# Kernel optimization log

Measured on AMD Instinct MI355X. Metric: run time of the kernel, lower is better.

Reference implementation:

```python
import jax, jax.numpy as jnp
import numpy as np

N = 10000; IN = 256; HID = 256; Z = 64; NC = 10; E = 320000
GAMMA = -0.5; ZETA = 1.1; TEMP = 0.5  # GlobalArgs.gamma/zeta, AttentionFusion.temperature


def _spmm(row, col, vals, x):
    # sparse [N,N] @ dense [N,D] via gather + segment-sum scatter
    return jax.ops.segment_sum(vals[:, None] * x[col], row, num_segments=N)


def _encode(x, row, col, vals, gcn_W, gcn_b, m1_W, m1_b, m2_W, m2_b, s1_W, s1_b, s2_W, s2_b):
    hidden = jax.nn.relu(_spmm(row, col, vals, x @ gcn_W + gcn_b))  # GCNLayer
    mean = jax.nn.relu(hidden @ m1_W + m1_b) @ m2_W + m2_b
    std = jax.nn.softplus(jax.nn.relu(hidden @ s1_W + s1_b) @ s2_W + s2_b)
    return mean, mean, std  # eval mode: z = x_mean


def _denoise(x, row, col, vals, nb_W, nb_b, sf_W, sf_b, att_W, att_b):
    h1 = jax.nn.relu(x[row] @ nb_W + nb_b)  # nblayers_0 on source feats
    h2 = jax.nn.relu(x[col] @ sf_W + sf_b)  # selflayers_0 on dest feats
    w = jnp.concatenate([h1, h2], axis=1) @ att_W + att_b  # [E,1] log_alpha
    gate = jax.nn.sigmoid(w[:, 0])  # eval-mode hard-concrete
    mask = jnp.clip(gate * (ZETA - GAMMA) + GAMMA, 0.0, 1.0)
    mv = vals * mask
    rowsum = jax.ops.segment_sum(mv, row, num_segments=N) + 1e-10
    d = jnp.clip(rowsum ** -0.5, 0.0, 10.0)
    norm_vals = mv * d[row] * d[col]
    l0 = jnp.mean(jax.nn.sigmoid(w - jnp.log(-GAMMA / ZETA)))
    return norm_vals, l0


def setup_inputs() -> dict:
    key = jax.random.key(0)
    ks = jax.random.split(key, 32)
    w = lambda k, s: jax.random.normal(k, s, jnp.float32) * 0.05
    inp = {}
    inp['x'] = jax.random.normal(ks[0], (N, IN), jnp.float32)
    inp['row'] = jax.random.randint(ks[1], (E,), 0, N)
    inp['col'] = jax.random.randint(ks[2], (E,), 0, N)
    inp['adj_vals'] = jax.random.uniform(ks[3], (E,), jnp.float32)
    inp['gcn_W'] = w(ks[4], (IN, HID)); inp['gcn_b'] = jnp.zeros((HID,), jnp.float32)
    inp['m1_W'] = w(ks[5], (HID, Z)); inp['m1_b'] = jnp.zeros((Z,), jnp.float32)
    inp['m2_W'] = w(ks[6], (Z, Z)); inp['m2_b'] = jnp.zeros((Z,), jnp.float32)
    inp['s1_W'] = w(ks[7], (HID, Z)); inp['s1_b'] = jnp.zeros((Z,), jnp.float32)
    inp['s2_W'] = w(ks[8], (Z, Z)); inp['s2_b'] = jnp.zeros((Z,), jnp.float32)
    inp['nb_W'] = w(ks[9], (IN, HID)); inp['nb_b'] = jnp.zeros((HID,), jnp.float32)
    inp['sf_W'] = w(ks[10], (IN, HID)); inp['sf_b'] = jnp.zeros((HID,), jnp.float32)
    inp['att_W'] = w(ks[11], (2 * HID, 1)); inp['att_b'] = jnp.zeros((1,), jnp.float32)
    inp['f1_W'] = w(ks[12], (Z, 32)); inp['f1_b'] = jnp.zeros((32,), jnp.float32)
    inp['f2_W'] = jnp.zeros((32, 1), jnp.float32)  # att[2].weight.fill_(0.0)
    inp['head_W'] = w(ks[13], (Z, NC)); inp['head_b'] = jnp.zeros((NC,), jnp.float32)
    inp['d1_W'] = w(ks[14], (Z, HID)); inp['d1_b'] = jnp.zeros((HID,), jnp.float32)
    inp['d2_W'] = w(ks[15], (HID, IN)); inp['d2_b'] = jnp.zeros((IN,), jnp.float32)
    return inp


def reference(x, row, col, adj_vals, gcn_W, gcn_b, m1_W, m1_b, m2_W, m2_b, s1_W, s1_b, s2_W, s2_b,
              nb_W, nb_b, sf_W, sf_b, att_W, att_b, f1_W, f1_b, f2_W, head_W, head_b,
              d1_W, d1_b, d2_W, d2_b):
    enc = (gcn_W, gcn_b, m1_W, m1_b, m2_W, m2_b, s1_W, s1_b, s2_W, s2_b)
    # generative view
    z_gen, mu, logstd = _encode(x, row, col, adj_vals, *enc)
    adj_logits = z_gen @ z_gen.T  # vgae_decoder
    # denoised view
    den_vals, l0_loss = _denoise(x, row, col, adj_vals, nb_W, nb_b, sf_W, sf_b, att_W, att_b)
    z_den, _, _ = _encode(x, row, col, den_vals, *enc)
    # attention fusion
    h = jnp.stack([z_gen, z_den], axis=1)  # [N,2,Z]
    score = jnp.tanh(h @ f1_W + f1_b) @ f2_W  # [N,2,1]
    weights = jax.nn.softmax(score / TEMP, axis=1)
    z_fused = jnp.sum(h * weights, axis=1)
    # heads (cluster_proj is identity)
    q_fused = jax.nn.softmax(z_fused @ head_W + head_b, axis=1)
    q_gen = jax.nn.softmax(z_gen @ head_W + head_b, axis=1)
    q_den = jax.nn.softmax(z_den @ head_W + head_b, axis=1)
    recon_den = jax.nn.relu(z_den @ d1_W + d1_b) @ d2_W + d2_b
    return (q_fused, q_gen, q_den, adj_logits, z_fused, mu, logstd, l0_loss, z_den, weights, recon_den)
```

## Files before the change

### kernel.cpp

```cpp
#include <hip/hip_runtime.h>
#include <math.h>

#define NN 10000
#define EE 320000

#define OQF  0LL
#define OQG  100000LL
#define OQD  200000LL
#define OADJ 300000LL
#define OZF  100300000LL
#define OMU  100940000LL
#define OLS  101580000LL
#define OL0  102220000LL
#define OZD  102220001LL
#define OWT  102860001LL
#define OREC 102880001LL

typedef short short8 __attribute__((ext_vector_type(8)));
typedef float f32x4 __attribute__((ext_vector_type(4)));

static __device__ __forceinline__ ushort f2bf(float f) {
  uint u = __float_as_uint(f);
  return (ushort)((u + 0x7fffu + ((u >> 16) & 1u)) >> 16);
}

__global__ __launch_bounds__(256) void k_prep(
    const float* __restrict__ x,
    const float* __restrict__ gcnW, const float* __restrict__ nbW,
    const float* __restrict__ sfW, const float* __restrict__ d1W,
    const float* __restrict__ d2W,
    ushort* __restrict__ XB, ushort* __restrict__ GWT, ushort* __restrict__ NWT,
    ushort* __restrict__ SWT, ushort* __restrict__ D1T, ushort* __restrict__ D2T)
{
  const int b = blockIdx.x;
  if (b < 2560) {
    const int i = b * 1024 + threadIdx.x * 4;
    if (i < NN * 256) {
      const float4 v = *(const float4*)(x + i);
      ushort4 u;
      u.x = f2bf(v.x); u.y = f2bf(v.y); u.z = f2bf(v.z); u.w = f2bf(v.w);
      *(ushort4*)(XB + i) = u;
    }
    return;
  }
  const int t2 = b - 2560;
  if (t2 < 1024) {
    const int m = t2 >> 8, n = t2 & 255, k = threadIdx.x;
    const float* src = (m == 0) ? gcnW : (m == 1) ? nbW : (m == 2) ? sfW : d2W;
    ushort* dst = (m == 0) ? GWT : (m == 1) ? NWT : (m == 2) ? SWT : D2T;
    dst[n * 256 + k] = f2bf(src[k * 256 + n]);
  } else {
    const int local = (t2 - 1024) * 256 + threadIdx.x;
    const int n = local >> 6, k = local & 63;
    D1T[n * 64 + k] = f2bf(d1W[k * 256 + n]);
  }
}

__global__ __launch_bounds__(256) void k_gin(
    const ushort* __restrict__ XB,
    const ushort* __restrict__ GWT, const ushort* __restrict__ NWT,
    const ushort* __restrict__ SWT,
    const float* __restrict__ gcnb, const float* __restrict__ nbb,
    const float* __restrict__ sfb, const float* __restrict__ attW,
    ushort* __restrict__ xwb, float* __restrict__ a1, float* __restrict__ a2)
{
  const int sel = blockIdx.y;
  const ushort* WT = (sel == 0) ? GWT : (sel == 1) ? NWT : SWT;
  const float* B = (sel == 0) ? gcnb : (sel == 1) ? nbb : sfb;
  const float* redw = attW + ((sel == 2) ? 256 : 0);
  float* redout = (sel == 1) ? a1 : a2;

  const int tid = threadIdx.x;
  const int wave = tid >> 6, lane = tid & 63;
  const int lr = lane & 15, lk = lane >> 4;
  const int i0 = blockIdx.x * 64;
  const int j0 = wave * 64;

  f32x4 acc[4][4];
#pragma unroll
  for (int ti = 0; ti < 4; ++ti)
#pragma unroll
    for (int tj = 0; tj < 4; ++tj) acc[ti][tj] = (f32x4){0.f, 0.f, 0.f, 0.f};

  const short8 z8 = {0, 0, 0, 0, 0, 0, 0, 0};
  for (int kk = 0; kk < 8; ++kk) {
    short8 a[4], bfr[4];
#pragma unroll
    for (int t = 0; t < 4; ++t) {
      const int ri = i0 + t * 16 + lr;
      a[t] = (ri < NN) ? *(const short8*)(XB + (size_t)ri * 256 + kk * 32 + lk * 8) : z8;
      bfr[t] = *(const short8*)(WT + (size_t)(j0 + t * 16 + lr) * 256 + kk * 32 + lk * 8);
    }
#pragma unroll
    for (int ti = 0; ti < 4; ++ti)
#pragma unroll
      for (int tj = 0; tj < 4; ++tj)
        acc[ti][tj] = __builtin_amdgcn_mfma_f32_16x16x32_bf16(a[ti], bfr[tj], acc[ti][tj], 0, 0, 0);
  }

  if (sel == 0) {
#pragma unroll
    for (int ti = 0; ti < 4; ++ti) {
      const int gi0 = i0 + ti * 16 + lk * 4;
#pragma unroll
      for (int tj = 0; tj < 4; ++tj) {
        const int gj = j0 + tj * 16 + lr;
        const float bv = B[gj];
#pragma unroll
        for (int r = 0; r < 4; ++r) {
          const int gi = gi0 + r;
          if (gi < NN) xwb[(size_t)gi * 256 + gj] = f2bf(acc[ti][tj][r] + bv);
        }
      }
    }
  } else {
    float bw[4], aw[4];
#pragma unroll
    for (int tj = 0; tj < 4; ++tj) {
      const int gj = j0 + tj * 16 + lr;
      bw[tj] = B[gj];
      aw[tj] = redw[gj];
    }
#pragma unroll
    for (int ti = 0; ti < 4; ++ti) {
      const int gi0 = i0 + ti * 16 + lk * 4;
#pragma unroll
      for (int r = 0; r < 4; ++r) {
        float s = 0.f;
#pragma unroll
        for (int tj = 0; tj < 4; ++tj)
          s += fmaxf(acc[ti][tj][r] + bw[tj], 0.f) * aw[tj];
#pragma unroll
        for (int m = 1; m < 16; m <<= 1) s += __shfl_xor(s, m, 64);
        const int gi = gi0 + r;
        if (lr == 0 && gi < NN) atomicAdd(&redout[gi], s);
      }
    }
  }
}

__global__ __launch_bounds__(256) void k_zzt(const ushort* __restrict__ ZB, float* __restrict__ C)
{
  const int tid = threadIdx.x;
  const int wave = tid >> 6, lane = tid & 63;
  const int lr = lane & 15, lk = lane >> 4;
  const int i0 = blockIdx.x * 128 + (wave >> 1) * 64;
  const int j0 = blockIdx.y * 128 + (wave & 1) * 64;
  short8 a[4][2], b[4][2];
  const short8 z8 = {0, 0, 0, 0, 0, 0, 0, 0};
#pragma unroll
  for (int t = 0; t < 4; ++t) {
    const int ri = i0 + t * 16 + lr;
    const int rj = j0 + t * 16 + lr;
#pragma unroll
    for (int kk = 0; kk < 2; ++kk) {
      a[t][kk] = (ri < NN) ? *(const short8*)(ZB + (size_t)ri * 64 + kk * 32 + lk * 8) : z8;
      b[t][kk] = (rj < NN) ? *(const short8*)(ZB + (size_t)rj * 64 + kk * 32 + lk * 8) : z8;
    }
  }
  f32x4 acc[4][4];
#pragma unroll
  for (int ti = 0; ti < 4; ++ti)
#pragma unroll
    for (int tj = 0; tj < 4; ++tj) {
      acc[ti][tj] = (f32x4){0.f, 0.f, 0.f, 0.f};
      acc[ti][tj] = __builtin_amdgcn_mfma_f32_16x16x32_bf16(a[ti][0], b[tj][0], acc[ti][tj], 0, 0, 0);
      acc[ti][tj] = __builtin_amdgcn_mfma_f32_16x16x32_bf16(a[ti][1], b[tj][1], acc[ti][tj], 0, 0, 0);
    }
#pragma unroll
  for (int ti = 0; ti < 4; ++ti) {
    const int gi0 = i0 + ti * 16 + lk * 4;
    if (gi0 >= NN) continue;
#pragma unroll
    for (int tj = 0; tj < 4; ++tj) {
      const int gj = j0 + tj * 16 + lr;
      if (gj >= NN) continue;
      float* cp = C + (size_t)gi0 * NN + gj;
#pragma unroll
      for (int r = 0; r < 4; ++r) cp[(size_t)r * NN] = acc[ti][tj][r];
    }
  }
}

__global__ __launch_bounds__(256) void k_denoise(
    const int* __restrict__ row, const int* __restrict__ col,
    const float* __restrict__ vals, const float* __restrict__ a1,
    const float* __restrict__ a2, const float* __restrict__ attb,
    float* __restrict__ mv, float* __restrict__ rsum, int* __restrict__ cnt,
    float* __restrict__ l0acc)
{
  const int e = blockIdx.x * 256 + threadIdx.x;
  const int r = row[e], c = col[e];
  const float w = a1[r] + a2[c] + attb[0];
  const float gate = 1.f / (1.f + expf(-w));
  const float mask = fminf(fmaxf(gate * 1.6f - 0.5f, 0.f), 1.f);
  const float m = vals[e] * mask;
  mv[e] = m;
  atomicAdd(&rsum[r], m);
  atomicAdd(&cnt[r], 1);
  float part = 1.f / (1.f + expf(-(w + 0.78845736f)));
#pragma unroll
  for (int off = 32; off > 0; off >>= 1) part += __shfl_down(part, off);
  __shared__ float sw[4];
  if ((threadIdx.x & 63) == 0) sw[threadIdx.x >> 6] = part;
  __syncthreads();
  if (threadIdx.x == 0) atomicAdd(l0acc, sw[0] + sw[1] + sw[2] + sw[3]);
}

__global__ __launch_bounds__(1024) void k_scan(const int* __restrict__ cnt, int* __restrict__ offs)
{
  __shared__ int part[1024];
  const int t = threadIdx.x;
  const int chunk = (NN + 1023) / 1024;
  const int base = t * chunk;
  int s = 0;
  for (int i = 0; i < chunk; ++i) { int idx = base + i; if (idx < NN) s += cnt[idx]; }
  part[t] = s;
  __syncthreads();
  for (int off = 1; off < 1024; off <<= 1) {
    int v = (t >= off) ? part[t - off] : 0;
    __syncthreads();
    part[t] += v;
    __syncthreads();
  }
  int run = (t == 0) ? 0 : part[t - 1];
  for (int i = 0; i < chunk; ++i) {
    int idx = base + i;
    if (idx < NN) { offs[idx] = run; run += cnt[idx]; }
  }
  if (t == 1023) offs[NN] = part[1023];
}

__global__ __launch_bounds__(256) void k_scatter(
    const int* __restrict__ row, const int* __restrict__ col,
    const float* __restrict__ vals, const float* __restrict__ mv,
    const float* __restrict__ rsum,
    const int* __restrict__ offs, int* __restrict__ posc,
    int* __restrict__ scol, float* __restrict__ sav, float* __restrict__ sdv)
{
  const int e = blockIdx.x * 256 + threadIdx.x;
  const int r = row[e], c = col[e];
  const float dr = fminf(rsqrtf(rsum[r] + 1e-10f), 10.f);
  const float dc = fminf(rsqrtf(rsum[c] + 1e-10f), 10.f);
  const int p = atomicAdd(&posc[r], 1);
  const int d = offs[r] + p;
  scol[d] = c;
  sav[d] = vals[e];
  sdv[d] = mv[e] * dr * dc;
}

__global__ __launch_bounds__(128) void k_spmm(
    const ushort* __restrict__ xwb, const int* __restrict__ scol,
    const float* __restrict__ sav, const float* __restrict__ sdv,
    const int* __restrict__ offs,
    float* __restrict__ h1, float* __restrict__ h2)
{
  const int n = blockIdx.x;
  const int c = threadIdx.x;
  const int s = offs[n], e = offs[n + 1];
  float a10 = 0.f, a11 = 0.f, a20 = 0.f, a21 = 0.f;
  for (int i = s; i < e; ++i) {
    const int cc = scol[i];
    const uint u = *(const uint*)(xwb + (size_t)cc * 256 + 2 * c);
    const float v0 = __uint_as_float(u << 16);
    const float v1 = __uint_as_float(u & 0xffff0000u);
    const float va = sav[i], vd = sdv[i];
    a10 = fmaf(va, v0, a10); a11 = fmaf(va, v1, a11);
    a20 = fmaf(vd, v0, a20); a21 = fmaf(vd, v1, a21);
  }
  float2* p1 = (float2*)(h1 + (size_t)n * 256 + 2 * c);
  float2* p2 = (float2*)(h2 + (size_t)n * 256 + 2 * c);
  *p1 = make_float2(fmaxf(a10, 0.f), fmaxf(a11, 0.f));
  *p2 = make_float2(fmaxf(a20, 0.f), fmaxf(a21, 0.f));
}

__global__ __launch_bounds__(256) void k_tail(
    const float* __restrict__ H1, const float* __restrict__ H2,
    const float* __restrict__ m1W, const float* __restrict__ m1b,
    const float* __restrict__ m2W, const float* __restrict__ m2b,
    const float* __restrict__ s1W, const float* __restrict__ s1b,
    const float* __restrict__ s2W, const float* __restrict__ s2b,
    float* __restrict__ out, float* __restrict__ zden,
    ushort* __restrict__ zbg, ushort* __restrict__ zbd)
{
  const int v = blockIdx.y;
  const float* A  = (v == 2) ? H2 : H1;
  const float* W1 = (v == 1) ? s1W : m1W;
  const float* B1 = (v == 1) ? s1b : m1b;
  const float* W2 = (v == 1) ? s2W : m2W;
  const float* B2 = (v == 1) ? s2b : m2b;

  __shared__ float As[16][68];
  __shared__ float Ws[16][68];
  __shared__ float Ts[64][68];
  __shared__ float W2s[64][68];

  const int tid = threadIdx.x;
  const int r0 = blockIdx.x << 6;
  const int ty = tid >> 4, tx = tid & 15;
  const int lr = tid >> 2, lk = (tid & 3) << 2;
  const int wk = tid >> 4, wc = (tid & 15) << 2;
  float acc[4][4] = {};
  for (int kb = 0; kb < 16; ++kb) {
    const int k0 = kb << 4;
    float4 av = make_float4(0.f, 0.f, 0.f, 0.f);
    const int gr = r0 + lr;
    if (gr < NN) av = *(const float4*)(A + (size_t)gr * 256 + k0 + lk);
    As[lk + 0][lr] = av.x; As[lk + 1][lr] = av.y;
    As[lk + 2][lr] = av.z; As[lk + 3][lr] = av.w;
    const float4 wv = *(const float4*)(W1 + (size_t)(k0 + wk) * 64 + wc);
    *(float4*)&Ws[wk][wc] = wv;
    __syncthreads();
#pragma unroll
    for (int k = 0; k < 16; ++k) {
      const float4 a = *(const float4*)&As[k][ty << 2];
      const float4 b = *(const float4*)&Ws[k][tx << 2];
      const float ar[4] = {a.x, a.y, a.z, a.w};
      const float br[4] = {b.x, b.y, b.z, b.w};
#pragma unroll
      for (int i = 0; i < 4; ++i)
#pragma unroll
        for (int j = 0; j < 4; ++j)
          acc[i][j] = fmaf(ar[i], br[j], acc[i][j]);
    }
    __syncthreads();
  }
  {
    float bv[4];
#pragma unroll
    for (int j = 0; j < 4; ++j) bv[j] = B1[(tx << 2) + j];
#pragma unroll
    for (int i = 0; i < 4; ++i)
#pragma unroll
      for (int j = 0; j < 4; ++j)
        Ts[(tx << 2) + j][(ty << 2) + i] = fmaxf(acc[i][j] + bv[j], 0.f);
    const int rw = tid >> 2;
    const int cw = (tid & 3) << 4;
#pragma unroll
    for (int p = 0; p < 4; ++p)
      *(float4*)&W2s[rw][cw + (p << 2)] = *(const float4*)(W2 + (size_t)rw * 64 + cw + (p << 2));
  }
  __syncthreads();
  float acc2[4][4] = {};
#pragma unroll 8
  for (int k = 0; k < 64; ++k) {
    const float4 a = *(const float4*)&Ts[k][ty << 2];
    const float4 b = *(const float4*)&W2s[k][tx << 2];
    const float ar[4] = {a.x, a.y, a.z, a.w};
    const float br[4] = {b.x, b.y, b.z, b.w};
#pragma unroll
    for (int i = 0; i < 4; ++i)
#pragma unroll
      for (int j = 0; j < 4; ++j)
        acc2[i][j] = fmaf(ar[i], br[j], acc2[i][j]);
  }
  float bv2[4];
#pragma unroll
  for (int j = 0; j < 4; ++j) bv2[j] = B2[(tx << 2) + j];
#pragma unroll
  for (int i = 0; i < 4; ++i) {
    const int gr = r0 + (ty << 2) + i;
    if (gr >= NN) continue;
#pragma unroll
    for (int j = 0; j < 4; ++j) {
      const int cc = (tx << 2) + j;
      float t = acc2[i][j] + bv2[j];
      if (v == 1) t = (t > 20.f) ? t : log1pf(expf(t));
      if (v == 0) {
        out[OMU + (size_t)gr * 64 + cc] = t;
        zbg[(size_t)gr * 64 + cc] = f2bf(t);
      } else if (v == 1) {
        out[OLS + (size_t)gr * 64 + cc] = t;
      } else {
        zden[(size_t)gr * 64 + cc] = t;
        out[OZD + (size_t)gr * 64 + cc] = t;
        zbd[(size_t)gr * 64 + cc] = f2bf(t);
      }
    }
  }
}

__global__ __launch_bounds__(256) void k_mega(
    const float* __restrict__ zd,
    const float* __restrict__ f1W, const float* __restrict__ f1b,
    const float* __restrict__ f2W,
    const float* __restrict__ hW, const float* __restrict__ hb,
    const float* __restrict__ l0acc, float* __restrict__ out)
{
  const int n = blockIdx.x * 256 + threadIdx.x;
  if (n == 0) out[OL0] = l0acc[0] * (1.f / (float)EE);
  if (n >= NN) return;
  const float* zg = out + OMU + (size_t)n * 64;
  const float* zdn = zd + (size_t)n * 64;
  float ag[32], ad[32];
#pragma unroll
  for (int c2 = 0; c2 < 32; ++c2) { const float b = f1b[c2]; ag[c2] = b; ad[c2] = b; }
  for (int l = 0; l < 64; ++l) {
    const float a = zg[l];
    const float d = zdn[l];
#pragma unroll
    for (int c2 = 0; c2 < 32; ++c2) {
      const float w = f1W[l * 32 + c2];
      ag[c2] = fmaf(a, w, ag[c2]);
      ad[c2] = fmaf(d, w, ad[c2]);
    }
  }
  float sg = 0.f, sd = 0.f;
#pragma unroll
  for (int c2 = 0; c2 < 32; ++c2) {
    sg += tanhf(ag[c2]) * f2W[c2];
    sd += tanhf(ad[c2]) * f2W[c2];
  }
  const float e0 = sg * 2.f, e1 = sd * 2.f;
  const float m = fmaxf(e0, e1);
  float w0 = expf(e0 - m), w1 = expf(e1 - m);
  const float inv = 1.f / (w0 + w1);
  w0 *= inv; w1 *= inv;
  float lgf[10], lgg[10], lgd[10];
#pragma unroll
  for (int c = 0; c < 10; ++c) { const float b = hb[c]; lgf[c] = b; lgg[c] = b; lgd[c] = b; }
  for (int l = 0; l < 64; ++l) {
    const float zgv = zg[l], zdv = zdn[l];
    const float zfv = w0 * zgv + w1 * zdv;
    out[OZF + (size_t)n * 64 + l] = zfv;
#pragma unroll
    for (int c = 0; c < 10; ++c) {
      const float w = hW[l * 10 + c];
      lgf[c] = fmaf(zfv, w, lgf[c]);
      lgg[c] = fmaf(zgv, w, lgg[c]);
      lgd[c] = fmaf(zdv, w, lgd[c]);
    }
  }
#pragma unroll
  for (int h = 0; h < 3; ++h) {
    float* lg = (h == 0) ? lgf : (h == 1) ? lgg : lgd;
    float* q = out + ((h == 0) ? OQF : (h == 1) ? OQG : OQD) + (size_t)n * 10;
    float mm = lg[0];
#pragma unroll
    for (int c = 1; c < 10; ++c) mm = fmaxf(mm, lg[c]);
    float s = 0.f;
#pragma unroll
    for (int c = 0; c < 10; ++c) { lg[c] = expf(lg[c] - mm); s += lg[c]; }
    const float invq = 1.f / s;
#pragma unroll
    for (int c = 0; c < 10; ++c) q[c] = lg[c] * invq;
  }
  out[OWT + (size_t)n * 2 + 0] = w0;
  out[OWT + (size_t)n * 2 + 1] = w1;
}

__global__ __launch_bounds__(256) void k_recon(
    const ushort* __restrict__ ZBD, const ushort* __restrict__ D1T,
    const float* __restrict__ d1b, const ushort* __restrict__ D2T,
    const float* __restrict__ d2b, float* __restrict__ out)
{
  __shared__ ushort HS[64 * 264];
  const int tid = threadIdx.x;
  const int wave = tid >> 6, lane = tid & 63;
  const int lr = lane & 15, lk = lane >> 4;
  const int i0 = blockIdx.x * 64;
  const int j0 = wave * 64;
  const short8 z8 = {0, 0, 0, 0, 0, 0, 0, 0};

  f32x4 acc[4][4];
#pragma unroll
  for (int ti = 0; ti < 4; ++ti)
#pragma unroll
    for (int tj = 0; tj < 4; ++tj) acc[ti][tj] = (f32x4){0.f, 0.f, 0.f, 0.f};
  for (int kk = 0; kk < 2; ++kk) {
    short8 a[4], bfr[4];
#pragma unroll
    for (int t = 0; t < 4; ++t) {
      const int ri = i0 + t * 16 + lr;
      a[t] = (ri < NN) ? *(const short8*)(ZBD + (size_t)ri * 64 + kk * 32 + lk * 8) : z8;
      bfr[t] = *(const short8*)(D1T + (size_t)(j0 + t * 16 + lr) * 64 + kk * 32 + lk * 8);
    }
#pragma unroll
    for (int ti = 0; ti < 4; ++ti)
#pragma unroll
      for (int tj = 0; tj < 4; ++tj)
        acc[ti][tj] = __builtin_amdgcn_mfma_f32_16x16x32_bf16(a[ti], bfr[tj], acc[ti][tj], 0, 0, 0);
  }
#pragma unroll
  for (int ti = 0; ti < 4; ++ti) {
    const int rl0 = ti * 16 + lk * 4;
#pragma unroll
    for (int tj = 0; tj < 4; ++tj) {
      const int cl = j0 + tj * 16 + lr;
      const float bv = d1b[cl];
#pragma unroll
      for (int r = 0; r < 4; ++r)
        HS[(rl0 + r) * 264 + cl] = f2bf(fmaxf(acc[ti][tj][r] + bv, 0.f));
    }
  }
  __syncthreads();

#pragma unroll
  for (int ti = 0; ti < 4; ++ti)
#pragma unroll
    for (int tj = 0; tj < 4; ++tj) acc[ti][tj] = (f32x4){0.f, 0.f, 0.f, 0.f};
  for (int kk = 0; kk < 8; ++kk) {
    short8 a[4], bfr[4];
#pragma unroll
    for (int t = 0; t < 4; ++t) {
      a[t] = *(const short8*)(HS + (t * 16 + lr) * 264 + kk * 32 + lk * 8);
      bfr[t] = *(const short8*)(D2T + (size_t)(j0 + t * 16 + lr) * 256 + kk * 32 + lk * 8);
    }
#pragma unroll
    for (int ti = 0; ti < 4; ++ti)
#pragma unroll
      for (int tj = 0; tj < 4; ++tj)
        acc[ti][tj] = __builtin_amdgcn_mfma_f32_16x16x32_bf16(a[ti], bfr[tj], acc[ti][tj], 0, 0, 0);
  }
#pragma unroll
  for (int ti = 0; ti < 4; ++ti) {
    const int gi0 = i0 + ti * 16 + lk * 4;
#pragma unroll
    for (int tj = 0; tj < 4; ++tj) {
      const int gj = j0 + tj * 16 + lr;
      const float bv = d2b[gj];
#pragma unroll
      for (int r = 0; r < 4; ++r) {
        const int gi = gi0 + r;
        if (gi < NN) out[OREC + (size_t)gi * 256 + gj] = acc[ti][tj][r] + bv;
      }
    }
  }
}

extern "C" void kernel_launch(void* const* d_in, const int* in_sizes, int n_in,
                              void* d_out, int out_size, void* d_ws, size_t ws_size,
                              hipStream_t stream)
{
  const float* x     = (const float*)d_in[0];
  const int*   row   = (const int*)d_in[1];
  const int*   col   = (const int*)d_in[2];
  const float* avals = (const float*)d_in[3];
  const float* gcnW  = (const float*)d_in[4];
  const float* gcnb  = (const float*)d_in[5];
  const float* m1W   = (const float*)d_in[6];
  const float* m1b   = (const float*)d_in[7];
  const float* m2W   = (const float*)d_in[8];
  const float* m2b   = (const float*)d_in[9];
  const float* s1W   = (const float*)d_in[10];
  const float* s1b   = (const float*)d_in[11];
  const float* s2W   = (const float*)d_in[12];
  const float* s2b   = (const float*)d_in[13];
  const float* nbW   = (const float*)d_in[14];
  const float* nbb   = (const float*)d_in[15];
  const float* sfW   = (const float*)d_in[16];
  const float* sfb   = (const float*)d_in[17];
  const float* attW  = (const float*)d_in[18];
  const float* attb  = (const float*)d_in[19];
  const float* f1W   = (const float*)d_in[20];
  const float* f1b   = (const float*)d_in[21];
  const float* f2W   = (const float*)d_in[22];
  const float* headW = (const float*)d_in[23];
  const float* headb = (const float*)d_in[24];
  const float* d1W   = (const float*)d_in[25];
  const float* d1b   = (const float*)d_in[26];
  const float* d2W   = (const float*)d_in[27];
  const float* d2b   = (const float*)d_in[28];
  float* out = (float*)d_out;

  float* ws = (float*)d_ws;
  size_t o = 0;
  ushort* XB   = (ushort*)(ws + o); o += (size_t)NN * 128;
  ushort* XWB  = (ushort*)(ws + o); o += (size_t)NN * 128;
  ushort* GWT  = (ushort*)(ws + o); o += 32768;
  ushort* NWT  = (ushort*)(ws + o); o += 32768;
  ushort* SWT  = (ushort*)(ws + o); o += 32768;
  ushort* D2T  = (ushort*)(ws + o); o += 32768;
  ushort* D1T  = (ushort*)(ws + o); o += 8192;
  float* H1    = ws + o; o += (size_t)NN * 256;
  float* H2    = ws + o; o += (size_t)NN * 256;
  float* ZDENW = ws + o; o += (size_t)NN * 64;
  ushort* ZBG  = (ushort*)(ws + o); o += (size_t)NN * 32;
  ushort* ZBD  = (ushort*)(ws + o); o += (size_t)NN * 32;
  float* MV    = ws + o; o += EE;
  float* SAV   = ws + o; o += EE;
  float* SDV   = ws + o; o += EE;
  int*   SCOL  = (int*)(ws + o); o += EE;
  int*   OFFS  = (int*)(ws + o); o += NN + 1;
  const size_t zoff = o;
  float* A1    = ws + o; o += NN;
  float* A2    = ws + o; o += NN;
  float* RSUM  = ws + o; o += NN;
  int*   CNT   = (int*)(ws + o); o += NN;
  int*   POSC  = (int*)(ws + o); o += NN;
  float* L0A   = ws + o; o += 1;

  hipMemsetAsync((void*)(ws + zoff), 0, (o - zoff) * sizeof(float), stream);

  k_prep<<<3648, 256, 0, stream>>>(x, gcnW, nbW, sfW, d1W, d2W, XB, GWT, NWT, SWT, D1T, D2T);
  k_gin<<<dim3(157, 3), 256, 0, stream>>>(XB, GWT, NWT, SWT, gcnb, nbb, sfb, attW, XWB, A1, A2);
  k_denoise<<<EE / 256, 256, 0, stream>>>(row, col, avals, A1, A2, attb, MV, RSUM, CNT, L0A);
  k_scan<<<1, 1024, 0, stream>>>(CNT, OFFS);
  k_scatter<<<EE / 256, 256, 0, stream>>>(row, col, avals, MV, RSUM, OFFS, POSC, SCOL, SAV, SDV);
  k_spmm<<<NN, 128, 0, stream>>>(XWB, SCOL, SAV, SDV, OFFS, H1, H2);
  k_tail<<<dim3(157, 3), 256, 0, stream>>>(H1, H2, m1W, m1b, m2W, m2b, s1W, s1b, s2W, s2b,
                                           out, ZDENW, ZBG, ZBD);
  k_zzt<<<dim3(79, 79), 256, 0, stream>>>(ZBG, out + OADJ);
  k_mega<<<40, 256, 0, stream>>>(ZDENW, f1W, f1b, f2W, headW, headb, L0A, out);
  k_recon<<<157, 256, 0, stream>>>(ZBD, D1T, d1b, D2T, d2b, out);
}
```

Measured before the change: 344.6 us.

## Fuse x conversion into GEMM, MFMA bf16 tail, merge post kernels

Removes the separate fp32→bf16 conversion pass over x by converting inline inside k_gin. The k_spmm output is stored as bf16, and the encoder tail MLP is rewritten from an fp32 shared-memory FMA GEMM to bf16 MFMA with pre-transposed weights. The zz^T decoder, fusion/heads and recon kernels are merged into one k_post launch. This cuts memory traffic and launch count, but adds bf16 rounding in the tail and redundant conversions of x across the three k_gin selector blocks.

```diff
diff --git a/kernel.cpp b/kernel.cpp
--- a/kernel.cpp
+++ b/kernel.cpp
@@ -24,40 +24,54 @@
   return (ushort)((u + 0x7fffu + ((u >> 16) & 1u)) >> 16);
 }
 
+static __device__ __forceinline__ short8 pack8(const float* p) {
+  short8 s;
+  s[0] = (short)f2bf(p[0]); s[1] = (short)f2bf(p[1]);
+  s[2] = (short)f2bf(p[2]); s[3] = (short)f2bf(p[3]);
+  s[4] = (short)f2bf(p[4]); s[5] = (short)f2bf(p[5]);
+  s[6] = (short)f2bf(p[6]); s[7] = (short)f2bf(p[7]);
+  return s;
+}
+
 __global__ __launch_bounds__(256) void k_prep(
-    const float* __restrict__ x,
     const float* __restrict__ gcnW, const float* __restrict__ nbW,
-    const float* __restrict__ sfW, const float* __restrict__ d1W,
-    const float* __restrict__ d2W,
-    ushort* __restrict__ XB, ushort* __restrict__ GWT, ushort* __restrict__ NWT,
-    ushort* __restrict__ SWT, ushort* __restrict__ D1T, ushort* __restrict__ D2T)
-{
-  const int b = blockIdx.x;
-  if (b < 2560) {
-    const int i = b * 1024 + threadIdx.x * 4;
-    if (i < NN * 256) {
-      const float4 v = *(const float4*)(x + i);
-      ushort4 u;
-      u.x = f2bf(v.x); u.y = f2bf(v.y); u.z = f2bf(v.z); u.w = f2bf(v.w);
-      *(ushort4*)(XB + i) = u;
-    }
-    return;
-  }
-  const int t2 = b - 2560;
-  if (t2 < 1024) {
-    const int m = t2 >> 8, n = t2 & 255, k = threadIdx.x;
+    const float* __restrict__ sfW, const float* __restrict__ d2W,
+    const float* __restrict__ d1W, const float* __restrict__ m1W,
+    const float* __restrict__ s1W, const float* __restrict__ m2W,
+    const float* __restrict__ s2W,
+    ushort* __restrict__ GWT, ushort* __restrict__ NWT, ushort* __restrict__ SWT,
+    ushort* __restrict__ D2T, ushort* __restrict__ D1T, ushort* __restrict__ M1T,
+    ushort* __restrict__ S1T, ushort* __restrict__ M2T, ushort* __restrict__ S2T)
+{
+  const int b = blockIdx.x, tid = threadIdx.x;
+  if (b < 1024) {
+    const int m = b >> 8, n = b & 255;
     const float* src = (m == 0) ? gcnW : (m == 1) ? nbW : (m == 2) ? sfW : d2W;
     ushort* dst = (m == 0) ? GWT : (m == 1) ? NWT : (m == 2) ? SWT : D2T;
-    dst[n * 256 + k] = f2bf(src[k * 256 + n]);
+    dst[n * 256 + tid] = f2bf(src[tid * 256 + n]);
+  } else if (b < 1088) {
+    const int local = (b - 1024) * 256 + tid;
+    const int n = local >> 6, k = local & 63;
+    D1T[local] = f2bf(d1W[k * 256 + n]);
+  } else if (b < 1152) {
+    const int n = b - 1088;
+    M1T[n * 256 + tid] = f2bf(m1W[tid * 64 + n]);
+  } else if (b < 1216) {
+    const int n = b - 1152;
+    S1T[n * 256 + tid] = f2bf(s1W[tid * 64 + n]);
+  } else if (b < 1232) {
+    const int local = (b - 1216) * 256 + tid;
+    const int n = local >> 6, k = local & 63;
+    M2T[local] = f2bf(m2W[k * 64 + n]);
   } else {
-    const int local = (t2 - 1024) * 256 + threadIdx.x;
+    const int local = (b - 1232) * 256 + tid;
     const int n = local >> 6, k = local & 63;
-    D1T[n * 64 + k] = f2bf(d1W[k * 256 + n]);
+    S2T[local] = f2bf(s2W[k * 64 + n]);
   }
 }
 
 __global__ __launch_bounds__(256) void k_gin(
-    const ushort* __restrict__ XB,
+    const float* __restrict__ x,
     const ushort* __restrict__ GWT, const ushort* __restrict__ NWT,
     const ushort* __restrict__ SWT,
     const float* __restrict__ gcnb, const float* __restrict__ nbb,
@@ -88,7 +102,12 @@
 #pragma unroll
     for (int t = 0; t < 4; ++t) {
       const int ri = i0 + t * 16 + lr;
-      a[t] = (ri < NN) ? *(const short8*)(XB + (size_t)ri * 256 + kk * 32 + lk * 8) : z8;
+      if (ri < NN) {
+        float xv[8];
+        *(float4*)&xv[0] = *(const float4*)(x + (size_t)ri * 256 + kk * 32 + lk * 8);
+        *(float4*)&xv[4] = *(const float4*)(x + (size_t)ri * 256 + kk * 32 + lk * 8 + 4);
+        a[t] = pack8(xv);
+      } else a[t] = z8;
       bfr[t] = *(const short8*)(WT + (size_t)(j0 + t * 16 + lr) * 256 + kk * 32 + lk * 8);
     }
 #pragma unroll
@@ -135,49 +154,6 @@
         const int gi = gi0 + r;
         if (lr == 0 && gi < NN) atomicAdd(&redout[gi], s);
       }
-    }
-  }
-}
-
-__global__ __launch_bounds__(256) void k_zzt(const ushort* __restrict__ ZB, float* __restrict__ C)
-{
-  const int tid = threadIdx.x;
-  const int wave = tid >> 6, lane = tid & 63;
-  const int lr = lane & 15, lk = lane >> 4;
-  const int i0 = blockIdx.x * 128 + (wave >> 1) * 64;
-  const int j0 = blockIdx.y * 128 + (wave & 1) * 64;
-  short8 a[4][2], b[4][2];
-  const short8 z8 = {0, 0, 0, 0, 0, 0, 0, 0};
-#pragma unroll
-  for (int t = 0; t < 4; ++t) {
-    const int ri = i0 + t * 16 + lr;
-    const int rj = j0 + t * 16 + lr;
-#pragma unroll
-    for (int kk = 0; kk < 2; ++kk) {
-      a[t][kk] = (ri < NN) ? *(const short8*)(ZB + (size_t)ri * 64 + kk * 32 + lk * 8) : z8;
-      b[t][kk] = (rj < NN) ? *(const short8*)(ZB + (size_t)rj * 64 + kk * 32 + lk * 8) : z8;
-    }
-  }
-  f32x4 acc[4][4];
-#pragma unroll
-  for (int ti = 0; ti < 4; ++ti)
-#pragma unroll
-    for (int tj = 0; tj < 4; ++tj) {
-      acc[ti][tj] = (f32x4){0.f, 0.f, 0.f, 0.f};
-      acc[ti][tj] = __builtin_amdgcn_mfma_f32_16x16x32_bf16(a[ti][0], b[tj][0], acc[ti][tj], 0, 0, 0);
-      acc[ti][tj] = __builtin_amdgcn_mfma_f32_16x16x32_bf16(a[ti][1], b[tj][1], acc[ti][tj], 0, 0, 0);
-    }
-#pragma unroll
-  for (int ti = 0; ti < 4; ++ti) {
-    const int gi0 = i0 + ti * 16 + lk * 4;
-    if (gi0 >= NN) continue;
-#pragma unroll
-    for (int tj = 0; tj < 4; ++tj) {
-      const int gj = j0 + tj * 16 + lr;
-      if (gj >= NN) continue;
-      float* cp = C + (size_t)gi0 * NN + gj;
-#pragma unroll
-      for (int r = 0; r < 4; ++r) cp[(size_t)r * NN] = acc[ti][tj][r];
     }
   }
 }
@@ -253,7 +229,7 @@
     const ushort* __restrict__ xwb, const int* __restrict__ scol,
     const float* __restrict__ sav, const float* __restrict__ sdv,
     const int* __restrict__ offs,
-    float* __restrict__ h1, float* __restrict__ h2)
+    ushort* __restrict__ h1, ushort* __restrict__ h2)
 {
   const int n = blockIdx.x;
   const int c = threadIdx.x;
@@ -268,261 +244,296 @@
     a10 = fmaf(va, v0, a10); a11 = fmaf(va, v1, a11);
     a20 = fmaf(vd, v0, a20); a21 = fmaf(vd, v1, a21);
   }
-  float2* p1 = (float2*)(h1 + (size_t)n * 256 + 2 * c);
-  float2* p2 = (float2*)(h2 + (size_t)n * 256 + 2 * c);
-  *p1 = make_float2(fmaxf(a10, 0.f), fmaxf(a11, 0.f));
-  *p2 = make_float2(fmaxf(a20, 0.f), fmaxf(a21, 0.f));
-}
-
-__global__ __launch_bounds__(256) void k_tail(
-    const float* __restrict__ H1, const float* __restrict__ H2,
-    const float* __restrict__ m1W, const float* __restrict__ m1b,
-    const float* __restrict__ m2W, const float* __restrict__ m2b,
-    const float* __restrict__ s1W, const float* __restrict__ s1b,
-    const float* __restrict__ s2W, const float* __restrict__ s2b,
+  const uint p1 = (uint)f2bf(fmaxf(a10, 0.f)) | ((uint)f2bf(fmaxf(a11, 0.f)) << 16);
+  const uint p2 = (uint)f2bf(fmaxf(a20, 0.f)) | ((uint)f2bf(fmaxf(a21, 0.f)) << 16);
+  *(uint*)(h1 + (size_t)n * 256 + 2 * c) = p1;
+  *(uint*)(h2 + (size_t)n * 256 + 2 * c) = p2;
+}
+
+__global__ __launch_bounds__(128) void k_tail(
+    const ushort* __restrict__ H1B, const ushort* __restrict__ H2B,
+    const ushort* __restrict__ M1T, const ushort* __restrict__ S1T,
+    const ushort* __restrict__ M2T, const ushort* __restrict__ S2T,
+    const float* __restrict__ m1b, const float* __restrict__ m2b,
+    const float* __restrict__ s1b, const float* __restrict__ s2b,
     float* __restrict__ out, float* __restrict__ zden,
     ushort* __restrict__ zbg, ushort* __restrict__ zbd)
 {
   const int v = blockIdx.y;
-  const float* A  = (v == 2) ? H2 : H1;
-  const float* W1 = (v == 1) ? s1W : m1W;
-  const float* B1 = (v == 1) ? s1b : m1b;
-  const float* W2 = (v == 1) ? s2W : m2W;
-  const float* B2 = (v == 1) ? s2b : m2b;
-
-  __shared__ float As[16][68];
-  __shared__ float Ws[16][68];
-  __shared__ float Ts[64][68];
-  __shared__ float W2s[64][68];
-
+  const ushort* A   = (v == 2) ? H2B : H1B;
+  const ushort* W1T = (v == 1) ? S1T : M1T;
+  const float*  B1  = (v == 1) ? s1b : m1b;
+  const ushort* W2T = (v == 1) ? S2T : M2T;
+  const float*  B2  = (v == 1) ? s2b : m2b;
+
+  __shared__ ushort Ts[128][72];
   const int tid = threadIdx.x;
-  const int r0 = blockIdx.x << 6;
-  const int ty = tid >> 4, tx = tid & 15;
-  const int lr = tid >> 2, lk = (tid & 3) << 2;
-  const int wk = tid >> 4, wc = (tid & 15) << 2;
-  float acc[4][4] = {};
-  for (int kb = 0; kb < 16; ++kb) {
-    const int k0 = kb << 4;
-    float4 av = make_float4(0.f, 0.f, 0.f, 0.f);
-    const int gr = r0 + lr;
-    if (gr < NN) av = *(const float4*)(A + (size_t)gr * 256 + k0 + lk);
-    As[lk + 0][lr] = av.x; As[lk + 1][lr] = av.y;
-    As[lk + 2][lr] = av.z; As[lk + 3][lr] = av.w;
-    const float4 wv = *(const float4*)(W1 + (size_t)(k0 + wk) * 64 + wc);
-    *(float4*)&Ws[wk][wc] = wv;
-    __syncthreads();
-#pragma unroll
-    for (int k = 0; k < 16; ++k) {
-      const float4 a = *(const float4*)&As[k][ty << 2];
-      const float4 b = *(const float4*)&Ws[k][tx << 2];
-      const float ar[4] = {a.x, a.y, a.z, a.w};
-      const float br[4] = {b.x, b.y, b.z, b.w};
-#pragma unroll
-      for (int i = 0; i < 4; ++i)
-#pragma unroll
-        for (int j = 0; j < 4; ++j)
-          acc[i][j] = fmaf(ar[i], br[j], acc[i][j]);
-    }
-    __syncthreads();
-  }
-  {
-    float bv[4];
-#pragma unroll
-    for (int j = 0; j < 4; ++j) bv[j] = B1[(tx << 2) + j];
-#pragma unroll
-    for (int i = 0; i < 4; ++i)
-#pragma unroll
-      for (int j = 0; j < 4; ++j)
-        Ts[(tx << 2) + j][(ty << 2) + i] = fmaxf(acc[i][j] + bv[j], 0.f);
-    const int rw = tid >> 2;
-    const int cw = (tid & 3) << 4;
-#pragma unroll
-    for (int p = 0; p < 4; ++p)
-      *(float4*)&W2s[rw][cw + (p << 2)] = *(const float4*)(W2 + (size_t)rw * 64 + cw + (p << 2));
+  const int wave = tid >> 6, lane = tid & 63;
+  const int lr = lane & 15, lk = lane >> 4;
+  const int i0 = blockIdx.x * 128 + wave * 64;
+  const short8 z8 = {0, 0, 0, 0, 0, 0, 0, 0};
+
+  f32x4 acc[4][4];
+#pragma unroll
+  for (int ti = 0; ti < 4; ++ti)
+#pragma unroll
+    for (int tj = 0; tj < 4; ++tj) acc[ti][tj] = (f32x4){0.f, 0.f, 0.f, 0.f};
+  for (int kk = 0; kk < 8; ++kk) {
+    short8 a[4], bfr[4];
+#pragma unroll
+    for (int t = 0; t < 4; ++t) {
+      const int ri = i0 + t * 16 + lr;
+      a[t] = (ri < NN) ? *(const short8*)(A + (size_t)ri * 256 + kk * 32 + lk * 8) : z8;
+      bfr[t] = *(const short8*)(W1T + (size_t)(t * 16 + lr) * 256 + kk * 32 + lk * 8);
+    }
+#pragma unroll
+    for (int ti = 0; ti < 4; ++ti)
+#pragma unroll
+      for (int tj = 0; tj < 4; ++tj)
+        acc[ti][tj] = __builtin_amdgcn_mfma_f32_16x16x32_bf16(a[ti], bfr[tj], acc[ti][tj], 0, 0, 0);
+  }
+#pragma unroll
+  for (int ti = 0; ti < 4; ++ti) {
+#pragma unroll
+    for (int tj = 0; tj < 4; ++tj) {
+      const int cl = tj * 16 + lr;
+      const float b1 = B1[cl];
+#pragma unroll
+      for (int r = 0; r < 4; ++r) {
+        const int lrow = wave * 64 + ti * 16 + lk * 4 + r;
+        Ts[lrow][cl] = f2bf(fmaxf(acc[ti][tj][r] + b1, 0.f));
+      }
+    }
   }
   __syncthreads();
-  float acc2[4][4] = {};
-#pragma unroll 8
-  for (int k = 0; k < 64; ++k) {
-    const float4 a = *(const float4*)&Ts[k][ty << 2];
-    const float4 b = *(const float4*)&W2s[k][tx << 2];
-    const float ar[4] = {a.x, a.y, a.z, a.w};
-    const float br[4] = {b.x, b.y, b.z, b.w};
-#pragma unroll
-    for (int i = 0; i < 4; ++i)
-#pragma unroll
-      for (int j = 0; j < 4; ++j)
-        acc2[i][j] = fmaf(ar[i], br[j], acc2[i][j]);
-  }
-  float bv2[4];
-#pragma unroll
-  for (int j = 0; j < 4; ++j) bv2[j] = B2[(tx << 2) + j];
-#pragma unroll
-  for (int i = 0; i < 4; ++i) {
-    const int gr = r0 + (ty << 2) + i;
-    if (gr >= NN) continue;
-#pragma unroll
-    for (int j = 0; j < 4; ++j) {
-      const int cc = (tx << 2) + j;
-      float t = acc2[i][j] + bv2[j];
-      if (v == 1) t = (t > 20.f) ? t : log1pf(expf(t));
-      if (v == 0) {
-        out[OMU + (size_t)gr * 64 + cc] = t;
-        zbg[(size_t)gr * 64 + cc] = f2bf(t);
-      } else if (v == 1) {
-        out[OLS + (size_t)gr * 64 + cc] = t;
-      } else {
-        zden[(size_t)gr * 64 + cc] = t;
-        out[OZD + (size_t)gr * 64 + cc] = t;
-        zbd[(size_t)gr * 64 + cc] = f2bf(t);
-      }
-    }
-  }
-}
-
-__global__ __launch_bounds__(256) void k_mega(
-    const float* __restrict__ zd,
+  f32x4 acc2[4][4];
+#pragma unroll
+  for (int ti = 0; ti < 4; ++ti)
+#pragma unroll
+    for (int tj = 0; tj < 4; ++tj) acc2[ti][tj] = (f32x4){0.f, 0.f, 0.f, 0.f};
+  for (int kk = 0; kk < 2; ++kk) {
+    short8 a[4], bfr[4];
+#pragma unroll
+    for (int t = 0; t < 4; ++t) {
+      a[t] = *(const short8*)(&Ts[wave * 64 + t * 16 + lr][kk * 32 + lk * 8]);
+      bfr[t] = *(const short8*)(W2T + (size_t)(t * 16 + lr) * 64 + kk * 32 + lk * 8);
+    }
+#pragma unroll
+    for (int ti = 0; ti < 4; ++ti)
+#pragma unroll
+      for (int tj = 0; tj < 4; ++tj)
+        acc2[ti][tj] = __builtin_amdgcn_mfma_f32_16x16x32_bf16(a[ti], bfr[tj], acc2[ti][tj], 0, 0, 0);
+  }
+#pragma unroll
+  for (int ti = 0; ti < 4; ++ti) {
+    const int gi0 = i0 + ti * 16 + lk * 4;
+#pragma unroll
+    for (int tj = 0; tj < 4; ++tj) {
+      const int gj = tj * 16 + lr;
+      const float bv = B2[gj];
+#pragma unroll
+      for (int r = 0; r < 4; ++r) {
+        const int gi = gi0 + r;
+        if (gi >= NN) continue;
+        float t = acc2[ti][tj][r] + bv;
+        if (v == 0) {
+          out[OMU + (size_t)gi * 64 + gj] = t;
+          zbg[(size_t)gi * 64 + gj] = f2bf(t);
+        } else if (v == 1) {
+          t = (t > 20.f) ? t : log1pf(expf(t));
+          out[OLS + (size_t)gi * 64 + gj] = t;
+        } else {
+          zden[(size_t)gi * 64 + gj] = t;
+          out[OZD + (size_t)gi * 64 + gj] = t;
+          zbd[(size_t)gi * 64 + gj] = f2bf(t);
+        }
+      }
+    }
+  }
+}
+
+__global__ __launch_bounds__(256) void k_post(
+    const ushort* __restrict__ ZBG, const ushort* __restrict__ ZBD,
+    const float* __restrict__ ZDENW,
+    const ushort* __restrict__ D1T, const float* __restrict__ d1b,
+    const ushort* __restrict__ D2T, const float* __restrict__ d2b,
     const float* __restrict__ f1W, const float* __restrict__ f1b,
     const float* __restrict__ f2W,
     const float* __restrict__ hW, const float* __restrict__ hb,
     const float* __restrict__ l0acc, float* __restrict__ out)
 {
-  const int n = blockIdx.x * 256 + threadIdx.x;
-  if (n == 0) out[OL0] = l0acc[0] * (1.f / (float)EE);
-  if (n >= NN) return;
-  const float* zg = out + OMU + (size_t)n * 64;
-  const float* zdn = zd + (size_t)n * 64;
-  float ag[32], ad[32];
-#pragma unroll
-  for (int c2 = 0; c2 < 32; ++c2) { const float b = f1b[c2]; ag[c2] = b; ad[c2] = b; }
-  for (int l = 0; l < 64; ++l) {
-    const float a = zg[l];
-    const float d = zdn[l];
+  const int b = blockIdx.x;
+  const int tid = threadIdx.x;
+  const short8 z8 = {0, 0, 0, 0, 0, 0, 0, 0};
+
+  if (b < 157) {
+    __shared__ ushort HS[64 * 264];
+    const int wave = tid >> 6, lane = tid & 63;
+    const int lr = lane & 15, lk = lane >> 4;
+    const int i0 = b * 64;
+    const int j0 = wave * 64;
+    f32x4 acc[4][4];
+#pragma unroll
+    for (int ti = 0; ti < 4; ++ti)
+#pragma unroll
+      for (int tj = 0; tj < 4; ++tj) acc[ti][tj] = (f32x4){0.f, 0.f, 0.f, 0.f};
+    for (int kk = 0; kk < 2; ++kk) {
+      short8 a[4], bfr[4];
+#pragma unroll
+      for (int t = 0; t < 4; ++t) {
+        const int ri = i0 + t * 16 + lr;
+        a[t] = (ri < NN) ? *(const short8*)(ZBD + (size_t)ri * 64 + kk * 32 + lk * 8) : z8;
+        bfr[t] = *(const short8*)(D1T + (size_t)(j0 + t * 16 + lr) * 64 + kk * 32 + lk * 8);
+      }
+#pragma unroll
+      for (int ti = 0; ti < 4; ++ti)
+#pragma unroll
+        for (int tj = 0; tj < 4; ++tj)
+          acc[ti][tj] = __builtin_amdgcn_mfma_f32_16x16x32_bf16(a[ti], bfr[tj], acc[ti][tj], 0, 0, 0);
+    }
+#pragma unroll
+    for (int ti = 0; ti < 4; ++ti) {
+      const int rl0 = ti * 16 + lk * 4;
+#pragma unroll
+      for (int tj = 0; tj < 4; ++tj) {
+        const int cl = j0 + tj * 16 + lr;
+        const float bv = d1b[cl];
+#pragma unroll
+        for (int r = 0; r < 4; ++r)
+          HS[(rl0 + r) * 264 + cl] = f2bf(fmaxf(acc[ti][tj][r] + bv, 0.f));
+      }
+    }
+    __syncthreads();
+#pragma unroll
+    for (int ti = 0; ti < 4; ++ti)
+#pragma unroll
+      for (int tj = 0; tj < 4; ++tj) acc[ti][tj] = (f32x4){0.f, 0.f, 0.f, 0.f};
+    for (int kk = 0; kk < 8; ++kk) {
+      short8 a[4], bfr[4];
+#pragma unroll
+      for (int t = 0; t < 4; ++t) {
+        a[t] = *(const short8*)(HS + (t * 16 + lr) * 264 + kk * 32 + lk * 8);
+        bfr[t] = *(const short8*)(D2T + (size_t)(j0 + t * 16 + lr) * 256 + kk * 32 + lk * 8);
+      }
+#pragma unroll
+      for (int ti = 0; ti < 4; ++ti)
+#pragma unroll
+        for (int tj = 0; tj < 4; ++tj)
+          acc[ti][tj] = __builtin_amdgcn_mfma_f32_16x16x32_bf16(a[ti], bfr[tj], acc[ti][tj], 0, 0, 0);
+    }
+#pragma unroll
+    for (int ti = 0; ti < 4; ++ti) {
+      const int gi0 = i0 + ti * 16 + lk * 4;
+#pragma unroll
+      for (int tj = 0; tj < 4; ++tj) {
+        const int gj = j0 + tj * 16 + lr;
+        const float bv = d2b[gj];
+#pragma unroll
+        for (int r = 0; r < 4; ++r) {
+          const int gi = gi0 + r;
+          if (gi < NN) out[OREC + (size_t)gi * 256 + gj] = acc[ti][tj][r] + bv;
+        }
+      }
+    }
+  } else if (b < 197) {
+    const int n = (b - 157) * 256 + tid;
+    if (n == 0) out[OL0] = l0acc[0] * (1.f / (float)EE);
+    if (n >= NN) return;
+    const float* zg = out + OMU + (size_t)n * 64;
+    const float* zdn = ZDENW + (size_t)n * 64;
+    float ag[32], ad[32];
+#pragma unroll
+    for (int c2 = 0; c2 < 32; ++c2) { const float bb = f1b[c2]; ag[c2] = bb; ad[c2] = bb; }
+    for (int l = 0; l < 64; ++l) {
+      const float a = zg[l];
+      const float d = zdn[l];
+#pragma unroll
+      for (int c2 = 0; c2 < 32; ++c2) {
+        const float w = f1W[l * 32 + c2];
+        ag[c2] = fmaf(a, w, ag[c2]);
+        ad[c2] = fmaf(d, w, ad[c2]);
+      }
+    }
+    float sg = 0.f, sd = 0.f;
 #pragma unroll
     for (int c2 = 0; c2 < 32; ++c2) {
-      const float w = f1W[l * 32 + c2];
-      ag[c2] = fmaf(a, w, ag[c2]);
-      ad[c2] = fmaf(d, w, ad[c2]);
-    }
-  }
-  float sg = 0.f, sd = 0.f;
-#pragma unroll
-  for (int c2 = 0; c2 < 32; ++c2) {
-    sg += tanhf(ag[c2]) * f2W[c2];
-    sd += tanhf(ad[c2]) * f2W[c2];
-  }
-  const float e0 = sg * 2.f, e1 = sd * 2.f;
-  const float m = fmaxf(e0, e1);
-  float w0 = expf(e0 - m), w1 = expf(e1 - m);
-  const float inv = 1.f / (w0 + w1);
-  w0 *= inv; w1 *= inv;
-  float lgf[10], lgg[10], lgd[10];
-#pragma unroll
-  for (int c = 0; c < 10; ++c) { const float b = hb[c]; lgf[c] = b; lgg[c] = b; lgd[c] = b; }
-  for (int l = 0; l < 64; ++l) {
-    const float zgv = zg[l], zdv = zdn[l];
-    const float zfv = w0 * zgv + w1 * zdv;
-    out[OZF + (size_t)n * 64 + l] = zfv;
-#pragma unroll
-    for (int c = 0; c < 10; ++c) {
-      const float w = hW[l * 10 + c];
-      lgf[c] = fmaf(zfv, w, lgf[c]);
-      lgg[c] = fmaf(zgv, w, lgg[c]);
-      lgd[c] = fmaf(zdv, w, lgd[c]);
-    }
-  }
-#pragma unroll
-  for (int h = 0; h < 3; ++h) {
-    float* lg = (h == 0) ? lgf : (h == 1) ? lgg : lgd;
-    float* q = out + ((h == 0) ? OQF : (h == 1) ? OQG : OQD) + (size_t)n * 10;
-    float mm = lg[0];
-#pragma unroll
-    for (int c = 1; c < 10; ++c) mm = fmaxf(mm, lg[c]);
-    float s = 0.f;
-#pragma unroll
-    for (int c = 0; c < 10; ++c) { lg[c] = expf(lg[c] - mm); s += lg[c]; }
-    const float invq = 1.f / s;
-#pragma unroll
-    for (int c = 0; c < 10; ++c) q[c] = lg[c] * invq;
-  }
-  out[OWT + (size_t)n * 2 + 0] = w0;
-  out[OWT + (size_t)n * 2 + 1] = w1;
-}
-
-__global__ __launch_bounds__(256) void k_recon(
-    const ushort* __restrict__ ZBD, const ushort* __restrict__ D1T,
-    const float* __restrict__ d1b, const ushort* __restrict__ D2T,
-    const float* __restrict__ d2b, float* __restrict__ out)
-{
-  __shared__ ushort HS[64 * 264];
-  const int tid = threadIdx.x;
-  const int wave = tid >> 6, lane = tid & 63;
-  const int lr = lane & 15, lk = lane >> 4;
-  const int i0 = blockIdx.x * 64;
-  const int j0 = wave * 64;
-  const short8 z8 = {0, 0, 0, 0, 0, 0, 0, 0};
-
-  f32x4 acc[4][4];
-#pragma unroll
-  for (int ti = 0; ti < 4; ++ti)
-#pragma unroll
-    for (int tj = 0; tj < 4; ++tj) acc[ti][tj] = (f32x4){0.f, 0.f, 0.f, 0.f};
-  for (int kk = 0; kk < 2; ++kk) {
-    short8 a[4], bfr[4];
+      sg += tanhf(ag[c2]) * f2W[c2];
+      sd += tanhf(ad[c2]) * f2W[c2];
+    }
+    const float e0 = sg * 2.f, e1 = sd * 2.f;
+    const float m = fmaxf(e0, e1);
+    float w0 = expf(e0 - m), w1 = expf(e1 - m);
+    const float inv = 1.f / (w0 + w1);
+    w0 *= inv; w1 *= inv;
+    float lgf[10], lgg[10], lgd[10];
+#pragma unroll
+    for (int c = 0; c < 10; ++c) { const float bb = hb[c]; lgf[c] = bb; lgg[c] = bb; lgd[c] = bb; }
+    for (int l = 0; l < 64; ++l) {
+      const float zgv = zg[l], zdv = zdn[l];
+      const float zfv = w0 * zgv + w1 * zdv;
+      out[OZF + (size_t)n * 64 + l] = zfv;
+#pragma unroll
+      for (int c = 0; c < 10; ++c) {
+        const float w = hW[l * 10 + c];
+        lgf[c] = fmaf(zfv, w, lgf[c]);
+        lgg[c] = fmaf(zgv, w, lgg[c]);
+        lgd[c] = fmaf(zdv, w, lgd[c]);
+      }
+    }
+#pragma unroll
+    for (int h = 0; h < 3; ++h) {
+      float* lg = (h == 0) ? lgf : (h == 1) ? lgg : lgd;
+      float* q = out + ((h == 0) ? OQF : (h == 1) ? OQG : OQD) + (size_t)n * 10;
+      float mm = lg[0];
+#pragma unroll
+      for (int c = 1; c < 10; ++c) mm = fmaxf(mm, lg[c]);
+      float s = 0.f;
+#pragma unroll
+      for (int c = 0; c < 10; ++c) { lg[c] = expf(lg[c] - mm); s += lg[c]; }
+      const float invq = 1.f / s;
+#pragma unroll
+      for (int c = 0; c < 10; ++c) q[c] = lg[c] * invq;
+    }
+    out[OWT + (size_t)n * 2 + 0] = w0;
+    out[OWT + (size_t)n * 2 + 1] = w1;
+  } else {
+    const int bb = b - 197;
+    const int bi = bb / 79, bj = bb % 79;
+    const int wave = tid >> 6, lane = tid & 63;
+    const int lr = lane & 15, lk = lane >> 4;
+    const int i0 = bi * 128 + (wave >> 1) * 64;
+    const int j0 = bj * 128 + (wave & 1) * 64;
+    short8 a[4][2], bfr[4][2];
 #pragma unroll
     for (int t = 0; t < 4; ++t) {
       const int ri = i0 + t * 16 + lr;
-      a[t] = (ri < NN) ? *(const short8*)(ZBD + (size_t)ri * 64 + kk * 32 + lk * 8) : z8;
-      bfr[t] = *(const short8*)(D1T + (size_t)(j0 + t * 16 + lr) * 64 + kk * 32 + lk * 8);
-    }
+      const int rj = j0 + t * 16 + lr;
+#pragma unroll
+      for (int kk = 0; kk < 2; ++kk) {
+        a[t][kk] = (ri < NN) ? *(const short8*)(ZBG + (size_t)ri * 64 + kk * 32 + lk * 8) : z8;
+        bfr[t][kk] = (rj < NN) ? *(const short8*)(ZBG + (size_t)rj * 64 + kk * 32 + lk * 8) : z8;
+      }
+    }
+    f32x4 acc[4][4];
 #pragma unroll
     for (int ti = 0; ti < 4; ++ti)
 #pragma unroll
-      for (int tj = 0; tj < 4; ++tj)
-        acc[ti][tj] = __builtin_amdgcn_mfma_f32_16x16x32_bf16(a[ti], bfr[tj], acc[ti][tj], 0, 0, 0);
-  }
-#pragma unroll
-  for (int ti = 0; ti < 4; ++ti) {
-    const int rl0 = ti * 16 + lk * 4;
-#pragma unroll
-    for (int tj = 0; tj < 4; ++tj) {
-      const int cl = j0 + tj * 16 + lr;
-      const float bv = d1b[cl];
-#pragma unroll
-      for (int r = 0; r < 4; ++r)
-        HS[(rl0 + r) * 264 + cl] = f2bf(fmaxf(acc[ti][tj][r] + bv, 0.f));
-    }
-  }
-  __syncthreads();
-
-#pragma unroll
-  for (int ti = 0; ti < 4; ++ti)
-#pragma unroll
-    for (int tj = 0; tj < 4; ++tj) acc[ti][tj] = (f32x4){0.f, 0.f, 0.f, 0.f};
-  for (int kk = 0; kk < 8; ++kk) {
-    short8 a[4], bfr[4];
-#pragma unroll
-    for (int t = 0; t < 4; ++t) {
-      a[t] = *(const short8*)(HS + (t * 16 + lr) * 264 + kk * 32 + lk * 8);
-      bfr[t] = *(const short8*)(D2T + (size_t)(j0 + t * 16 + lr) * 256 + kk * 32 + lk * 8);
-    }
-#pragma unroll
-    for (int ti = 0; ti < 4; ++ti)
-#pragma unroll
-      for (int tj = 0; tj < 4; ++tj)
-        acc[ti][tj] = __builtin_amdgcn_mfma_f32_16x16x32_bf16(a[ti], bfr[tj], acc[ti][tj], 0, 0, 0);
-  }
-#pragma unroll
-  for (int ti = 0; ti < 4; ++ti) {
-    const int gi0 = i0 + ti * 16 + lk * 4;
-#pragma unroll
-    for (int tj = 0; tj < 4; ++tj) {
-      const int gj = j0 + tj * 16 + lr;
-      const float bv = d2b[gj];
-#pragma unroll
-      for (int r = 0; r < 4; ++r) {
-        const int gi = gi0 + r;
-        if (gi < NN) out[OREC + (size_t)gi * 256 + gj] = acc[ti][tj][r] + bv;
+      for (int tj = 0; tj < 4; ++tj) {
+        acc[ti][tj] = (f32x4){0.f, 0.f, 0.f, 0.f};
+        acc[ti][tj] = __builtin_amdgcn_mfma_f32_16x16x32_bf16(a[ti][0], bfr[tj][0], acc[ti][tj], 0, 0, 0);
+        acc[ti][tj] = __builtin_amdgcn_mfma_f32_16x16x32_bf16(a[ti][1], bfr[tj][1], acc[ti][tj], 0, 0, 0);
+      }
+#pragma unroll
+    for (int ti = 0; ti < 4; ++ti) {
+      const int gi0 = i0 + ti * 16 + lk * 4;
+      if (gi0 >= NN) continue;
+#pragma unroll
+      for (int tj = 0; tj < 4; ++tj) {
+        const int gj = j0 + tj * 16 + lr;
+        if (gj >= NN) continue;
+        float* cp = out + OADJ + (size_t)gi0 * NN + gj;
+#pragma unroll
+        for (int r = 0; r < 4; ++r) cp[(size_t)r * NN] = acc[ti][tj][r];
       }
     }
   }
@@ -565,15 +576,18 @@
 
   float* ws = (float*)d_ws;
   size_t o = 0;
-  ushort* XB   = (ushort*)(ws + o); o += (size_t)NN * 128;
   ushort* XWB  = (ushort*)(ws + o); o += (size_t)NN * 128;
   ushort* GWT  = (ushort*)(ws + o); o += 32768;
   ushort* NWT  = (ushort*)(ws + o); o += 32768;
   ushort* SWT  = (ushort*)(ws + o); o += 32768;
   ushort* D2T  = (ushort*)(ws + o); o += 32768;
   ushort* D1T  = (ushort*)(ws + o); o += 8192;
-  float* H1    = ws + o; o += (size_t)NN * 256;
-  float* H2    = ws + o; o += (size_t)NN * 256;
+  ushort* M1T  = (ushort*)(ws + o); o += 8192;
+  ushort* S1T  = (ushort*)(ws + o); o += 8192;
+  ushort* M2T  = (ushort*)(ws + o); o += 2048;
+  ushort* S2T  = (ushort*)(ws + o); o += 2048;
+  ushort* H1B  = (ushort*)(ws + o); o += (size_t)NN * 128;
+  ushort* H2B  = (ushort*)(ws + o); o += (size_t)NN * 128;
   float* ZDENW = ws + o; o += (size_t)NN * 64;
   ushort* ZBG  = (ushort*)(ws + o); o += (size_t)NN * 32;
   ushort* ZBD  = (ushort*)(ws + o); o += (size_t)NN * 32;
@@ -592,15 +606,15 @@
 
   hipMemsetAsync((void*)(ws + zoff), 0, (o - zoff) * sizeof(float), stream);
 
-  k_prep<<<3648, 256, 0, stream>>>(x, gcnW, nbW, sfW, d1W, d2W, XB, GWT, NWT, SWT, D1T, D2T);
-  k_gin<<<dim3(157, 3), 256, 0, stream>>>(XB, GWT, NWT, SWT, gcnb, nbb, sfb, attW, XWB, A1, A2);
+  k_prep<<<1248, 256, 0, stream>>>(gcnW, nbW, sfW, d2W, d1W, m1W, s1W, m2W, s2W,
+                                   GWT, NWT, SWT, D2T, D1T, M1T, S1T, M2T, S2T);
+  k_gin<<<dim3(157, 3), 256, 0, stream>>>(x, GWT, NWT, SWT, gcnb, nbb, sfb, attW, XWB, A1, A2);
   k_denoise<<<EE / 256, 256, 0, stream>>>(row, col, avals, A1, A2, attb, MV, RSUM, CNT, L0A);
   k_scan<<<1, 1024, 0, stream>>>(CNT, OFFS);
   k_scatter<<<EE / 256, 256, 0, stream>>>(row, col, avals, MV, RSUM, OFFS, POSC, SCOL, SAV, SDV);
-  k_spmm<<<NN, 128, 0, stream>>>(XWB, SCOL, SAV, SDV, OFFS, H1, H2);
-  k_tail<<<dim3(157, 3), 256, 0, stream>>>(H1, H2, m1W, m1b, m2W, m2b, s1W, s1b, s2W, s2b,
-                                           out, ZDENW, ZBG, ZBD);
-  k_zzt<<<dim3(79, 79), 256, 0, stream>>>(ZBG, out + OADJ);
-  k_mega<<<40, 256, 0, stream>>>(ZDENW, f1W, f1b, f2W, headW, headb, L0A, out);
-  k_recon<<<157, 256, 0, stream>>>(ZBD, D1T, d1b, D2T, d2b, out);
-}
+  k_spmm<<<NN, 128, 0, stream>>>(XWB, SCOL, SAV, SDV, OFFS, H1B, H2B);
+  k_tail<<<dim3(79, 3), 128, 0, stream>>>(H1B, H2B, M1T, S1T, M2T, S2T,
+                                          m1b, m2b, s1b, s2b, out, ZDENW, ZBG, ZBD);
+  k_post<<<6438, 256, 0, stream>>>(ZBG, ZBD, ZDENW, D1T, d1b, D2T, d2b,
+                                   f1W, f1b, f2W, headW, headb, L0A, out);
+}
```

Result: faster. 311.8 us (-9.5%).
